# Kernel tuning notes

Measured on AMD Instinct MI355X. Metric: run time of the kernel, lower is better.

## Reference

```python
import jax, jax.numpy as jnp
import numpy as np

B, M, T, L, K = 64, 16, 2048, 64, 32
N = T - L + 1  # 1985 sliding-window positions


def setup_inputs() -> dict:
    key = jax.random.key(0)
    k1, k2, k3 = jax.random.split(key, 3)
    x = jax.random.normal(k1, (B, M, T), dtype=jnp.float32)
    # shapelets initialized uniform(-1, 1) as in nn.init.uniform_
    shapelets = jax.random.uniform(k2, (K, L), dtype=jnp.float32, minval=-1.0, maxval=1.0)
    # penalty maps (learned; zeros at init, random here for a non-trivial weighting)
    penalty_maps = 0.1 * jax.random.normal(k3, (K, M, N), dtype=jnp.float32)
    return {"x": x, "shapelets": shapelets, "penalty_maps": penalty_maps}


def reference(x, shapelets, penalty_maps):
    # x: (B, M, T); shapelets: (K, L); penalty_maps: (K, M, N)
    Lw = shapelets.shape[1]
    n_pos = x.shape[2] - Lw + 1
    # sliding-window view: (B, M, N, L), equivalent to torch unfold(dim=2, size=L, step=1)
    idx = jnp.arange(n_pos)[:, None] + jnp.arange(Lw)[None, :]
    sub = x[:, :, idx]  # (B, M, N, L)

    def per_shapelet(args):
        shp, pmap = args  # (L,), (M, N)
        # raw squared L2 distance over window, per channel/position: (B, M, N)
        raw = jnp.sum((sub - shp[None, None, None, :]) ** 2, axis=3)
        pen = jax.nn.elu(-pmap) + 2.0  # (M, N)
        wd = jnp.sum(raw * pen[None], axis=1)  # sum over channels -> (B, N)
        return jnp.min(wd, axis=1)  # min over positions -> (B,)

    # sequential map over the K shapelets avoids a Kx blow-up of the (B,M,N,L) intermediate
    feats = jax.lax.map(per_shapelet, (shapelets, penalty_maps))  # (K, B)
    return feats.T  # (B, K)
```

## Files before the change

kernel.cpp:

```cpp
#include <hip/hip_runtime.h>
#include <hip/hip_bf16.h>

#define B_ 64
#define M_ 16
#define T_ 2048
#define L_ 64
#define K_ 32
#define N_ (T_ - L_ + 1)
#define KMN (K_ * M_ * N_)
#define TN 64
#define NTH 256
#define NBSEQ 4
#define XROW 144
#define STSTR 72
#define SQSTR 64

typedef __attribute__((ext_vector_type(8))) short bf16x8;
typedef __attribute__((ext_vector_type(4))) float f32x4;

__device__ __forceinline__ unsigned short f2bf(float f) {
    __hip_bfloat16 h = __float2bfloat16(f);
    return __builtin_bit_cast(unsigned short, h);
}

__global__ void pen_init_kernel(const float* __restrict__ pmap,
                                const float* __restrict__ shp,
                                float* __restrict__ pen,
                                float* __restrict__ ss_ws,
                                unsigned* __restrict__ out) {
    const int gid = blockIdx.x * 256 + threadIdx.x;
    if (gid < B_ * K_) out[gid] = 0x7F800000u;
    if (gid < K_) {
        float s = 0.f;
        for (int l = 0; l < L_; ++l) { float v = shp[gid * L_ + l]; s = fmaf(v, v, s); }
        ss_ws[gid] = s;
    }
#pragma unroll
    for (int half = 0; half < 2; ++half) {
        const int item = gid + half * (KMN / 8);
        if (item < KMN / 4) {
            const int i4 = item * 4;
            float4 p = *(const float4*)(pmap + i4);
            float4 r;
            r.x = (p.x < 0.f) ? (2.f - p.x) : (__expf(-p.x) + 1.f);
            r.y = (p.y < 0.f) ? (2.f - p.y) : (__expf(-p.y) + 1.f);
            r.z = (p.z < 0.f) ? (2.f - p.z) : (__expf(-p.z) + 1.f);
            r.w = (p.w < 0.f) ? (2.f - p.w) : (__expf(-p.w) + 1.f);
            *(float4*)(pen + i4) = r;
        }
    }
}

__global__ __launch_bounds__(NTH, 2)
void shapelet_mfma_kernel(const float* __restrict__ x,
                          const float* __restrict__ shp,
                          const float* __restrict__ pen,
                          const float* __restrict__ ss_ws,
                          unsigned* __restrict__ out) {
    __shared__ __align__(16) unsigned short xbuf4[M_][4][XROW];
    __shared__ __align__(16) unsigned short st[K_][STSTR];
    __shared__ __align__(16) float sqw[M_][SQSTR];

    const int tid = threadIdx.x;
    const int bx = blockIdx.x;
    const int n0 = bx * TN;
    const bool fast = (n0 + 128 <= T_);

    const int lane = tid & 63;
    const int w  = tid >> 6;
    const int rl = lane & 15;
    const int q  = lane >> 4;
    const int sp = rl & 3;
    const int e0 = 16 * w + 8 * q + (rl & ~3);
    const int eq = e0 >> 2;
    const int nrow = n0 + 16 * w + 4 * q;

    for (int i = tid; i < K_ * 16; i += NTH) {
        const int k = i >> 4, l4 = (i & 15) * 4;
        float4 v = *(const float4*)(shp + k * L_ + l4);
        ushort4 sv = { f2bf(v.x), f2bf(v.y), f2bf(v.z), f2bf(v.w) };
        *(ushort4*)&st[k][l4] = sv;
    }
    const float ssk0 = ss_ws[rl], ssk1 = ss_ws[16 + rl];
    __syncthreads();

    bf16x8 bfr[2][2];
#pragma unroll
    for (int t = 0; t < 2; ++t)
#pragma unroll
        for (int h = 0; h < 2; ++h)
            bfr[t][h] = *(const bf16x8*)&st[16 * t + rl][8 * q + 32 * h];

    const float* pr0_base = pen + (size_t)rl * (M_ * N_) + nrow;
    const f32x4 zero = (f32x4)0.f;

    for (int bb = 0; bb < NBSEQ; ++bb) {
        const int b = blockIdx.y * NBSEQ + bb;

        const float* xb = x + ((size_t)b * M_) * T_ + n0;
        for (int g = tid; g < M_ * 31; g += NTH) {
            const int m = g / 31, j4 = (g - m * 31) * 4;
            const float* src = xb + m * T_ + j4;
            float h[8];
            if (fast) {
                float4 v0 = *(const float4*)src;
                float4 v1 = *(const float4*)(src + 4);
                h[0] = v0.x; h[1] = v0.y; h[2] = v0.z; h[3] = v0.w;
                h[4] = v1.x; h[5] = v1.y; h[6] = v1.z; h[7] = v1.w;
            } else {
#pragma unroll
                for (int i = 0; i < 8; ++i)
                    h[i] = (n0 + j4 + i < T_) ? src[i] : 0.f;
            }
            unsigned short hb[8];
#pragma unroll
            for (int i = 0; i < 8; ++i) hb[i] = f2bf(h[i]);
#pragma unroll
            for (int s = 0; s < 4; ++s) {
                ushort4 sv = { hb[s], hb[s + 1], hb[s + 2], hb[s + 3] };
                *(ushort4*)&xbuf4[m][s][j4] = sv;
            }
        }
        if (tid < M_ * 8) {
            const int m = tid >> 3, j0 = (tid & 7) * 8;
            const float* xr = x + ((size_t)b * M_ + m) * T_ + n0;
            float s = 0.f;
            if (fast) {
#pragma unroll
                for (int qd = 0; qd < 16; ++qd) {
                    float4 v = *(const float4*)(xr + j0 + qd * 4);
                    s = fmaf(v.x, v.x, s); s = fmaf(v.y, v.y, s);
                    s = fmaf(v.z, v.z, s); s = fmaf(v.w, v.w, s);
                }
                sqw[m][j0] = s;
#pragma unroll
                for (int d = 1; d < 8; ++d) {
                    float a = xr[j0 + d + L_ - 1], r = xr[j0 + d - 1];
                    s += a * a - r * r;
                    sqw[m][j0 + d] = s;
                }
            } else {
                for (int l = 0; l < L_; ++l) {
                    float v = (n0 + j0 + l < T_) ? xr[j0 + l] : 0.f;
                    s = fmaf(v, v, s);
                }
                sqw[m][j0] = s;
                for (int d = 1; d < 8; ++d) {
                    float a = (n0 + j0 + d + L_ - 1 < T_) ? xr[j0 + d + L_ - 1] : 0.f;
                    float r = (n0 + j0 + d - 1 < T_) ? xr[j0 + d - 1] : 0.f;
                    s += a * a - r * r;
                    sqw[m][j0 + d] = s;
                }
            }
        }
        __syncthreads();

        const float* pr0 = pr0_base;
        const float* pr1 = pr0 + (size_t)16 * M_ * N_;

        f32x4 wd0 = (f32x4)0.f, wd1 = (f32x4)0.f;

#pragma unroll 2
        for (int m = 0; m < M_; ++m) {
            float4 p0, p1;
            if (fast) {
                p0 = *(const float4*)(pr0 + (size_t)m * N_);
                p1 = *(const float4*)(pr1 + (size_t)m * N_);
            } else {
                p0 = make_float4(2.f, 2.f, 2.f, 2.f);
                p1 = make_float4(2.f, 2.f, 2.f, 2.f);
                const float* r0_ = pr0 + (size_t)m * N_;
                const float* r1_ = pr1 + (size_t)m * N_;
                if (nrow     < N_) { p0.x = r0_[0]; p1.x = r1_[0]; }
                if (nrow + 1 < N_) { p0.y = r0_[1]; p1.y = r1_[1]; }
                if (nrow + 2 < N_) { p0.z = r0_[2]; p1.z = r1_[2]; }
                if (nrow + 3 < N_) { p0.w = r0_[3]; p1.w = r1_[3]; }
            }

            const uint2* prow = (const uint2*)&xbuf4[m][sp][0];
            uint2 lo0 = prow[eq],     hi0 = prow[eq + 1];
            uint2 lo1 = prow[eq + 8], hi1 = prow[eq + 9];
            union { uint2 u2[2]; bf16x8 v; } fa0, fa1;
            fa0.u2[0] = lo0; fa0.u2[1] = hi0;
            fa1.u2[0] = lo1; fa1.u2[1] = hi1;

            f32x4 c0_ = __builtin_amdgcn_mfma_f32_16x16x32_bf16(fa0.v, bfr[0][0], zero, 0, 0, 0);
            c0_       = __builtin_amdgcn_mfma_f32_16x16x32_bf16(fa1.v, bfr[0][1], c0_, 0, 0, 0);
            f32x4 c1_ = __builtin_amdgcn_mfma_f32_16x16x32_bf16(fa0.v, bfr[1][0], zero, 0, 0, 0);
            c1_       = __builtin_amdgcn_mfma_f32_16x16x32_bf16(fa1.v, bfr[1][1], c1_, 0, 0, 0);

            f32x4 sq = *(const f32x4*)&sqw[m][16 * w + 4 * q];
            const float pe0[4] = { p0.x, p0.y, p0.z, p0.w };
            const float pe1[4] = { p1.x, p1.y, p1.z, p1.w };
#pragma unroll
            for (int r = 0; r < 4; ++r) {
                float t0v = fmaf(-2.f, c0_[r], sq[r] + ssk0);
                wd0[r] = fmaf(pe0[r], t0v, wd0[r]);
                float t1v = fmaf(-2.f, c1_[r], sq[r] + ssk1);
                wd1[r] = fmaf(pe1[r], t1v, wd1[r]);
            }
        }

        __syncthreads();
        float* red = (float*)&sqw[0][0];
#pragma unroll
        for (int t = 0; t < 2; ++t) {
            float lmin = __int_as_float(0x7F800000);
            const f32x4 wdv = t ? wd1 : wd0;
#pragma unroll
            for (int r = 0; r < 4; ++r)
                if (nrow + r < N_) lmin = fminf(lmin, wdv[r]);
            lmin = fminf(lmin, __shfl_xor(lmin, 16));
            lmin = fminf(lmin, __shfl_xor(lmin, 32));
            if (q == 0) red[w * 32 + t * 16 + rl] = lmin;
        }
        __syncthreads();
        if (tid < K_) {
            float v = fminf(fminf(red[tid], red[32 + tid]),
                            fminf(red[64 + tid], red[96 + tid]));
            atomicMin(out + (size_t)b * K_ + tid, __float_as_uint(fmaxf(v, 0.f)));
        }
        __syncthreads();
    }
}

extern "C" void kernel_launch(void* const* d_in, const int* in_sizes, int n_in,
                              void* d_out, int out_size, void* d_ws, size_t ws_size,
                              hipStream_t stream) {
    const float* x    = (const float*)d_in[0];
    const float* shp  = (const float*)d_in[1];
    const float* pmap = (const float*)d_in[2];
    unsigned* out = (unsigned*)d_out;
    float* pen   = (float*)d_ws;
    float* ss_ws = pen + KMN;

    pen_init_kernel<<<dim3((KMN / 8 + 255) / 256), dim3(256), 0, stream>>>(
        pmap, shp, pen, ss_ws, out);

    dim3 grid((N_ + TN - 1) / TN, B_ / NBSEQ);
    shapelet_mfma_kernel<<<grid, dim3(NTH), 0, stream>>>(x, shp, pen, ss_ws, out);
}
```

Before: 109.6 us.

## Split channel loop across two wave groups, one batch per block

Each block now handles a single batch element instead of looping over four, and uses 512 threads. The two groups of four waves each cover half of the 16 channels and combine their partial sums through shared memory before the min reduction. The aim is more parallelism and occupancy with a shorter serial channel loop per wave. The cost is a 4x larger grid, and shapelets are converted and penalty rows re-read once per batch rather than once per four batches. It also adds an extra LDS exchange and barrier per block.

```diff
diff --git a/kernel.cpp b/kernel.cpp
--- a/kernel.cpp
+++ b/kernel.cpp
@@ -9,8 +9,7 @@
 #define N_ (T_ - L_ + 1)
 #define KMN (K_ * M_ * N_)
 #define TN 64
-#define NTH 256
-#define NBSEQ 4
+#define NTH 512
 #define XROW 144
 #define STSTR 72
 #define SQSTR 64
@@ -51,7 +50,7 @@
     }
 }
 
-__global__ __launch_bounds__(NTH, 2)
+__global__ __launch_bounds__(NTH, 8)
 void shapelet_mfma_kernel(const float* __restrict__ x,
                           const float* __restrict__ shp,
                           const float* __restrict__ pen,
@@ -62,25 +61,84 @@
     __shared__ __align__(16) float sqw[M_][SQSTR];
 
     const int tid = threadIdx.x;
-    const int bx = blockIdx.x;
-    const int n0 = bx * TN;
+    const int n0 = blockIdx.x * TN;
+    const int b  = blockIdx.y;
     const bool fast = (n0 + 128 <= T_);
 
+    {
+        const int k = tid >> 4, l4 = (tid & 15) * 4;
+        float4 v = *(const float4*)(shp + k * L_ + l4);
+        ushort4 sv = { f2bf(v.x), f2bf(v.y), f2bf(v.z), f2bf(v.w) };
+        *(ushort4*)&st[k][l4] = sv;
+    }
+
+    const float* xb = x + ((size_t)b * M_) * T_ + n0;
+    if (tid < M_ * 31) {
+        const int m = tid / 31, j4 = (tid - m * 31) * 4;
+        const float* src = xb + m * T_ + j4;
+        float h[8];
+        if (fast) {
+            float4 v0 = *(const float4*)src;
+            float4 v1 = *(const float4*)(src + 4);
+            h[0] = v0.x; h[1] = v0.y; h[2] = v0.z; h[3] = v0.w;
+            h[4] = v1.x; h[5] = v1.y; h[6] = v1.z; h[7] = v1.w;
+        } else {
+#pragma unroll
+            for (int i = 0; i < 8; ++i)
+                h[i] = (n0 + j4 + i < T_) ? src[i] : 0.f;
+        }
+        unsigned short hb[8];
+#pragma unroll
+        for (int i = 0; i < 8; ++i) hb[i] = f2bf(h[i]);
+#pragma unroll
+        for (int s = 0; s < 4; ++s) {
+            ushort4 sv = { hb[s], hb[s + 1], hb[s + 2], hb[s + 3] };
+            *(ushort4*)&xbuf4[m][s][j4] = sv;
+        }
+    }
+    if (tid < M_ * 8) {
+        const int m = tid >> 3, j0 = (tid & 7) * 8;
+        const float* xr = x + ((size_t)b * M_ + m) * T_ + n0;
+        float s = 0.f;
+        if (fast) {
+#pragma unroll
+            for (int qd = 0; qd < 16; ++qd) {
+                float4 v = *(const float4*)(xr + j0 + qd * 4);
+                s = fmaf(v.x, v.x, s); s = fmaf(v.y, v.y, s);
+                s = fmaf(v.z, v.z, s); s = fmaf(v.w, v.w, s);
+            }
+            sqw[m][j0] = s;
+#pragma unroll
+            for (int d = 1; d < 8; ++d) {
+                float a = xr[j0 + d + L_ - 1], r = xr[j0 + d - 1];
+                s += a * a - r * r;
+                sqw[m][j0 + d] = s;
+            }
+        } else {
+            for (int l = 0; l < L_; ++l) {
+                float v = (n0 + j0 + l < T_) ? xr[j0 + l] : 0.f;
+                s = fmaf(v, v, s);
+            }
+            sqw[m][j0] = s;
+            for (int d = 1; d < 8; ++d) {
+                float a = (n0 + j0 + d + L_ - 1 < T_) ? xr[j0 + d + L_ - 1] : 0.f;
+                float r = (n0 + j0 + d - 1 < T_) ? xr[j0 + d - 1] : 0.f;
+                s += a * a - r * r;
+                sqw[m][j0 + d] = s;
+            }
+        }
+    }
+
     const int lane = tid & 63;
-    const int w  = tid >> 6;
+    const int wsub = (tid >> 6) & 3;
+    const int wg   = tid >> 8;
     const int rl = lane & 15;
     const int q  = lane >> 4;
     const int sp = rl & 3;
-    const int e0 = 16 * w + 8 * q + (rl & ~3);
+    const int e0 = 16 * wsub + 8 * q + (rl & ~3);
     const int eq = e0 >> 2;
-    const int nrow = n0 + 16 * w + 4 * q;
-
-    for (int i = tid; i < K_ * 16; i += NTH) {
-        const int k = i >> 4, l4 = (i & 15) * 4;
-        float4 v = *(const float4*)(shp + k * L_ + l4);
-        ushort4 sv = { f2bf(v.x), f2bf(v.y), f2bf(v.z), f2bf(v.w) };
-        *(ushort4*)&st[k][l4] = sv;
-    }
+    const int nrow = n0 + 16 * wsub + 4 * q;
+
     const float ssk0 = ss_ws[rl], ssk1 = ss_ws[16 + rl];
     __syncthreads();
 
@@ -91,117 +149,68 @@
         for (int h = 0; h < 2; ++h)
             bfr[t][h] = *(const bf16x8*)&st[16 * t + rl][8 * q + 32 * h];
 
-    const float* pr0_base = pen + (size_t)rl * (M_ * N_) + nrow;
+    const float* pr0 = pen + (size_t)rl * (M_ * N_) + nrow + (size_t)(8 * wg) * N_;
+    const float* pr1 = pr0 + (size_t)16 * M_ * N_;
+
+    f32x4 wd0 = (f32x4)0.f, wd1 = (f32x4)0.f;
     const f32x4 zero = (f32x4)0.f;
 
-    for (int bb = 0; bb < NBSEQ; ++bb) {
-        const int b = blockIdx.y * NBSEQ + bb;
-
-        const float* xb = x + ((size_t)b * M_) * T_ + n0;
-        for (int g = tid; g < M_ * 31; g += NTH) {
-            const int m = g / 31, j4 = (g - m * 31) * 4;
-            const float* src = xb + m * T_ + j4;
-            float h[8];
-            if (fast) {
-                float4 v0 = *(const float4*)src;
-                float4 v1 = *(const float4*)(src + 4);
-                h[0] = v0.x; h[1] = v0.y; h[2] = v0.z; h[3] = v0.w;
-                h[4] = v1.x; h[5] = v1.y; h[6] = v1.z; h[7] = v1.w;
-            } else {
-#pragma unroll
-                for (int i = 0; i < 8; ++i)
-                    h[i] = (n0 + j4 + i < T_) ? src[i] : 0.f;
-            }
-            unsigned short hb[8];
-#pragma unroll
-            for (int i = 0; i < 8; ++i) hb[i] = f2bf(h[i]);
-#pragma unroll
-            for (int s = 0; s < 4; ++s) {
-                ushort4 sv = { hb[s], hb[s + 1], hb[s + 2], hb[s + 3] };
-                *(ushort4*)&xbuf4[m][s][j4] = sv;
-            }
-        }
-        if (tid < M_ * 8) {
-            const int m = tid >> 3, j0 = (tid & 7) * 8;
-            const float* xr = x + ((size_t)b * M_ + m) * T_ + n0;
-            float s = 0.f;
-            if (fast) {
-#pragma unroll
-                for (int qd = 0; qd < 16; ++qd) {
-                    float4 v = *(const float4*)(xr + j0 + qd * 4);
-                    s = fmaf(v.x, v.x, s); s = fmaf(v.y, v.y, s);
-                    s = fmaf(v.z, v.z, s); s = fmaf(v.w, v.w, s);
-                }
-                sqw[m][j0] = s;
-#pragma unroll
-                for (int d = 1; d < 8; ++d) {
-                    float a = xr[j0 + d + L_ - 1], r = xr[j0 + d - 1];
-                    s += a * a - r * r;
-                    sqw[m][j0 + d] = s;
-                }
-            } else {
-                for (int l = 0; l < L_; ++l) {
-                    float v = (n0 + j0 + l < T_) ? xr[j0 + l] : 0.f;
-                    s = fmaf(v, v, s);
-                }
-                sqw[m][j0] = s;
-                for (int d = 1; d < 8; ++d) {
-                    float a = (n0 + j0 + d + L_ - 1 < T_) ? xr[j0 + d + L_ - 1] : 0.f;
-                    float r = (n0 + j0 + d - 1 < T_) ? xr[j0 + d - 1] : 0.f;
-                    s += a * a - r * r;
-                    sqw[m][j0 + d] = s;
-                }
-            }
-        }
-        __syncthreads();
-
-        const float* pr0 = pr0_base;
-        const float* pr1 = pr0 + (size_t)16 * M_ * N_;
-
-        f32x4 wd0 = (f32x4)0.f, wd1 = (f32x4)0.f;
-
 #pragma unroll 2
-        for (int m = 0; m < M_; ++m) {
-            float4 p0, p1;
-            if (fast) {
-                p0 = *(const float4*)(pr0 + (size_t)m * N_);
-                p1 = *(const float4*)(pr1 + (size_t)m * N_);
-            } else {
-                p0 = make_float4(2.f, 2.f, 2.f, 2.f);
-                p1 = make_float4(2.f, 2.f, 2.f, 2.f);
-                const float* r0_ = pr0 + (size_t)m * N_;
-                const float* r1_ = pr1 + (size_t)m * N_;
-                if (nrow     < N_) { p0.x = r0_[0]; p1.x = r1_[0]; }
-                if (nrow + 1 < N_) { p0.y = r0_[1]; p1.y = r1_[1]; }
-                if (nrow + 2 < N_) { p0.z = r0_[2]; p1.z = r1_[2]; }
-                if (nrow + 3 < N_) { p0.w = r0_[3]; p1.w = r1_[3]; }
-            }
-
-            const uint2* prow = (const uint2*)&xbuf4[m][sp][0];
-            uint2 lo0 = prow[eq],     hi0 = prow[eq + 1];
-            uint2 lo1 = prow[eq + 8], hi1 = prow[eq + 9];
-            union { uint2 u2[2]; bf16x8 v; } fa0, fa1;
-            fa0.u2[0] = lo0; fa0.u2[1] = hi0;
-            fa1.u2[0] = lo1; fa1.u2[1] = hi1;
-
-            f32x4 c0_ = __builtin_amdgcn_mfma_f32_16x16x32_bf16(fa0.v, bfr[0][0], zero, 0, 0, 0);
-            c0_       = __builtin_amdgcn_mfma_f32_16x16x32_bf16(fa1.v, bfr[0][1], c0_, 0, 0, 0);
-            f32x4 c1_ = __builtin_amdgcn_mfma_f32_16x16x32_bf16(fa0.v, bfr[1][0], zero, 0, 0, 0);
-            c1_       = __builtin_amdgcn_mfma_f32_16x16x32_bf16(fa1.v, bfr[1][1], c1_, 0, 0, 0);
-
-            f32x4 sq = *(const f32x4*)&sqw[m][16 * w + 4 * q];
-            const float pe0[4] = { p0.x, p0.y, p0.z, p0.w };
-            const float pe1[4] = { p1.x, p1.y, p1.z, p1.w };
-#pragma unroll
-            for (int r = 0; r < 4; ++r) {
-                float t0v = fmaf(-2.f, c0_[r], sq[r] + ssk0);
-                wd0[r] = fmaf(pe0[r], t0v, wd0[r]);
-                float t1v = fmaf(-2.f, c1_[r], sq[r] + ssk1);
-                wd1[r] = fmaf(pe1[r], t1v, wd1[r]);
-            }
-        }
-
-        __syncthreads();
+    for (int mm = 0; mm < M_ / 2; ++mm) {
+        const int m = 8 * wg + mm;
+        float4 p0, p1;
+        if (fast) {
+            p0 = *(const float4*)(pr0 + (size_t)mm * N_);
+            p1 = *(const float4*)(pr1 + (size_t)mm * N_);
+        } else {
+            p0 = make_float4(2.f, 2.f, 2.f, 2.f);
+            p1 = make_float4(2.f, 2.f, 2.f, 2.f);
+            const float* r0_ = pr0 + (size_t)mm * N_;
+            const float* r1_ = pr1 + (size_t)mm * N_;
+            if (nrow     < N_) { p0.x = r0_[0]; p1.x = r1_[0]; }
+            if (nrow + 1 < N_) { p0.y = r0_[1]; p1.y = r1_[1]; }
+            if (nrow + 2 < N_) { p0.z = r0_[2]; p1.z = r1_[2]; }
+            if (nrow + 3 < N_) { p0.w = r0_[3]; p1.w = r1_[3]; }
+        }
+
+        const uint2* prow = (const uint2*)&xbuf4[m][sp][0];
+        uint2 lo0 = prow[eq],     hi0 = prow[eq + 1];
+        uint2 lo1 = prow[eq + 8], hi1 = prow[eq + 9];
+        union { uint2 u2[2]; bf16x8 v; } fa0, fa1;
+        fa0.u2[0] = lo0; fa0.u2[1] = hi0;
+        fa1.u2[0] = lo1; fa1.u2[1] = hi1;
+
+        f32x4 c0_ = __builtin_amdgcn_mfma_f32_16x16x32_bf16(fa0.v, bfr[0][0], zero, 0, 0, 0);
+        c0_       = __builtin_amdgcn_mfma_f32_16x16x32_bf16(fa1.v, bfr[0][1], c0_, 0, 0, 0);
+        f32x4 c1_ = __builtin_amdgcn_mfma_f32_16x16x32_bf16(fa0.v, bfr[1][0], zero, 0, 0, 0);
+        c1_       = __builtin_amdgcn_mfma_f32_16x16x32_bf16(fa1.v, bfr[1][1], c1_, 0, 0, 0);
+
+        f32x4 sq = *(const f32x4*)&sqw[m][16 * wsub + 4 * q];
+        const float pe0[4] = { p0.x, p0.y, p0.z, p0.w };
+        const float pe1[4] = { p1.x, p1.y, p1.z, p1.w };
+#pragma unroll
+        for (int r = 0; r < 4; ++r) {
+            float t0v = fmaf(-2.f, c0_[r], sq[r] + ssk0);
+            wd0[r] = fmaf(pe0[r], t0v, wd0[r]);
+            float t1v = fmaf(-2.f, c1_[r], sq[r] + ssk1);
+            wd1[r] = fmaf(pe1[r], t1v, wd1[r]);
+        }
+    }
+
+    __syncthreads();
+    float* scr = (float*)&xbuf4[0][0][0];
+    if (wg == 1) {
+        float* dst = scr + ((wsub * 64 + lane) * 8);
+#pragma unroll
+        for (int r = 0; r < 4; ++r) { dst[r] = wd0[r]; dst[4 + r] = wd1[r]; }
+    }
+    __syncthreads();
+
+    if (wg == 0) {
+        const float* src = scr + ((wsub * 64 + lane) * 8);
+#pragma unroll
+        for (int r = 0; r < 4; ++r) { wd0[r] += src[r]; wd1[r] += src[4 + r]; }
+
         float* red = (float*)&sqw[0][0];
 #pragma unroll
         for (int t = 0; t < 2; ++t) {
@@ -212,15 +221,15 @@
                 if (nrow + r < N_) lmin = fminf(lmin, wdv[r]);
             lmin = fminf(lmin, __shfl_xor(lmin, 16));
             lmin = fminf(lmin, __shfl_xor(lmin, 32));
-            if (q == 0) red[w * 32 + t * 16 + rl] = lmin;
-        }
-        __syncthreads();
-        if (tid < K_) {
-            float v = fminf(fminf(red[tid], red[32 + tid]),
-                            fminf(red[64 + tid], red[96 + tid]));
-            atomicMin(out + (size_t)b * K_ + tid, __float_as_uint(fmaxf(v, 0.f)));
-        }
-        __syncthreads();
+            if (q == 0) red[wsub * 32 + t * 16 + rl] = lmin;
+        }
+    }
+    __syncthreads();
+    if (tid < K_) {
+        const float* red = (const float*)&sqw[0][0];
+        float v = fminf(fminf(red[tid], red[32 + tid]),
+                        fminf(red[64 + tid], red[96 + tid]));
+        atomicMin(out + (size_t)b * K_ + tid, __float_as_uint(fmaxf(v, 0.f)));
     }
 }
 
@@ -237,6 +246,6 @@
     pen_init_kernel<<<dim3((KMN / 8 + 255) / 256), dim3(256), 0, stream>>>(
         pmap, shp, pen, ss_ws, out);
 
-    dim3 grid((N_ + TN - 1) / TN, B_ / NBSEQ);
+    dim3 grid((N_ + TN - 1) / TN, B_);
     shapelet_mfma_kernel<<<grid, dim3(NTH), 0, stream>>>(x, shp, pen, ss_ws, out);
 }
```

Measured after the change: 115.6 us. 1.05x slower.
